# Performance work log

Hardware: AMD Instinct MI355X
Metric: run time of the kernel (lower is better)

The kernel has to match this reference:

```python
import jax, jax.numpy as jnp
import numpy as np

B, S, FEAT = 4, 512, 16
D, H, L, DFF, NC, RPH = 512, 8, 6, 2048, 12, 64
DH = D // H
CLAMP = 5.0
LN_EPS = 1e-5
STD_EPS = 1e-6


def setup_inputs() -> dict:
    key = jax.random.key(0)
    ks = iter(jax.random.split(key, 32))
    sc = lambda *shape: 0.02 * jax.random.normal(next(ks), shape, dtype=jnp.float32)
    inp = {
        "x": jax.random.normal(next(ks), (B, S, FEAT), dtype=jnp.float32),
        # RelPosBias2D MLP: Linear(2,RPH) -> ReLU -> Linear(RPH,H)
        "relpos_w1": sc(RPH, 2), "relpos_b1": jnp.zeros((RPH,), jnp.float32),
        "relpos_w2": sc(H, RPH), "relpos_b2": jnp.zeros((H,), jnp.float32),
        "embed_w": sc(D, FEAT), "embed_b": jnp.zeros((D,), jnp.float32),
        # per-layer params stacked on leading L axis
        "attn_in_w": sc(L, 3 * D, D), "attn_in_b": jnp.zeros((L, 3 * D), jnp.float32),
        "attn_out_w": sc(L, D, D), "attn_out_b": jnp.zeros((L, D), jnp.float32),
        "ff_w1": sc(L, DFF, D), "ff_b1": jnp.zeros((L, DFF), jnp.float32),
        "ff_w2": sc(L, D, DFF), "ff_b2": jnp.zeros((L, D), jnp.float32),
        "ln1_s": jnp.ones((L, D), jnp.float32), "ln1_b": jnp.zeros((L, D), jnp.float32),
        "ln2_s": jnp.ones((L, D), jnp.float32), "ln2_b": jnp.zeros((L, D), jnp.float32),
        "fc_w": sc(NC, D), "fc_b": jnp.zeros((NC,), jnp.float32),
    }
    return inp


def _standardize(v):  # (B,S), unmasked path of _masked_standardize
    mean = v.mean(axis=1, keepdims=True)
    var = ((v - mean) ** 2).mean(axis=1, keepdims=True)
    return (v - mean) / jnp.sqrt(var + STD_EPS)


def _layernorm(v, s, b):
    mean = v.mean(axis=-1, keepdims=True)
    var = ((v - mean) ** 2).mean(axis=-1, keepdims=True)
    return (v - mean) * jax.lax.rsqrt(var + LN_EPS) * s + b


def reference(x, relpos_w1, relpos_b1, relpos_w2, relpos_b2, embed_w, embed_b,
              attn_in_w, attn_in_b, attn_out_w, attn_out_b,
              ff_w1, ff_b1, ff_w2, ff_b2, ln1_s, ln1_b, ln2_s, ln2_b, fc_w, fc_b):
    # --- 2D relative position bias ---
    t = _standardize(x[..., 0])
    f = _standardize(x[..., 1])
    dt = t[:, :, None] - t[:, None, :]          # (B,S,S)
    df = f[:, :, None] - f[:, None, :]
    rel = jnp.stack([dt, df], axis=-1)           # (B,S,S,2)
    hid = jax.nn.relu(rel @ relpos_w1.T + relpos_b1)
    bias = hid @ relpos_w2.T + relpos_b2         # (B,S,S,H)
    bias = jnp.clip(bias, -CLAMP, CLAMP)
    bias = jnp.transpose(bias, (0, 3, 1, 2))     # (B,H,S,S)

    h = x @ embed_w.T + embed_b                  # (B,S,D)
    scale = 1.0 / jnp.sqrt(jnp.float32(DH))
    for l in range(L):
        qkv = h @ attn_in_w[l].T + attn_in_b[l]  # (B,S,3D)
        q, k, v = jnp.split(qkv, 3, axis=-1)
        q = q.reshape(B, S, H, DH)
        k = k.reshape(B, S, H, DH)
        v = v.reshape(B, S, H, DH)
        scores = jnp.einsum('bihd,bjhd->bhij', q, k) * scale + bias
        attn = jax.nn.softmax(scores, axis=-1)
        o = jnp.einsum('bhij,bjhd->bihd', attn, v).reshape(B, S, D)
        o = o @ attn_out_w[l].T + attn_out_b[l]
        h = _layernorm(h + o, ln1_s[l], ln1_b[l])
        ff = jax.nn.relu(h @ ff_w1[l].T + ff_b1[l]) @ ff_w2[l].T + ff_b2[l]
        h = _layernorm(h + ff, ln2_s[l], ln2_b[l])

    rep = h.mean(axis=1)                         # mean pooling, no mask
    return rep @ fc_w.T + fc_b                   # (B,NC)
```

## Files before the change

### kernel.cpp

```cpp
#include <hip/hip_runtime.h>
#include <hip/hip_bf16.h>
#include <stdint.h>

using short8 = __attribute__((ext_vector_type(8))) short;
using us4    = __attribute__((ext_vector_type(4))) unsigned short;
using f32x4  = __attribute__((ext_vector_type(4))) float;
using bf16   = __hip_bfloat16;

constexpr int CB=4, CS=512, CF=16, CD=512, CH=8, CL=6, CDFF=2048, CNC=12, CRPH=64, CDH=64;

__device__ inline void gload_lds16(const void* g, void* l) {
    __builtin_amdgcn_global_load_lds((const __attribute__((address_space(1))) void*)g,
                                     (__attribute__((address_space(3))) void*)l, 16, 0, 0);
}
__device__ inline float bfbits2f(unsigned short u) {
    return __uint_as_float(((uint32_t)u) << 16);
}
__device__ inline unsigned short f2bfbits(float f) {
    return __builtin_bit_cast(unsigned short, __float2bfloat16(f));
}

template<int BM, int BN, int TPB>
struct MMGeom {
    static constexpr int WC  = (TPB == 512) ? 4 : 2;
    static constexpr int WR  = (TPB/64)/WC;
    static constexpr int RS  = BM/WR;
    static constexpr int CSP = BN/WC;
    static constexpr int MR  = RS/16;
    static constexpr int NR  = CSP/16;
    static constexpr int NLD = (BM+BN)*128/(TPB*16);
};

template<int BM, int BN, int TPB>
__device__ inline void stage_tile(const bf16* A, int lda, const bf16* W, int ldw, int k0,
                                  char* As, char* Bs) {
    constexpr int AC = (BM*128)/(TPB*16);
    constexpr int BC = (BN*128)/(TPB*16);
    const int tid = threadIdx.x;
#pragma unroll
    for (int i = 0; i < AC; i++) {
        int s = i*TPB + tid;
        int r = s >> 3, u = s & 7;
        const char* gp = (const char*)(A + (size_t)r*lda + k0) + ((u ^ (r&7))*16);
        gload_lds16(gp, As + (size_t)(s & ~63)*16);
    }
#pragma unroll
    for (int i = 0; i < BC; i++) {
        int s = i*TPB + tid;
        int r = s >> 3, u = s & 7;
        const char* gp = (const char*)(W + (size_t)r*ldw + k0) + ((u ^ (r&7))*16);
        gload_lds16(gp, Bs + (size_t)(s & ~63)*16);
    }
}

template<int BM, int BN, int TPB>
__device__ inline void compute_tile64(const char* As, const char* Bs,
                                      int wr, int wc, int c, int g,
                                      f32x4 (&acc)[MMGeom<BM,BN,TPB>::MR][MMGeom<BM,BN,TPB>::NR]) {
    using G = MMGeom<BM,BN,TPB>;
#pragma unroll
    for (int kk = 0; kk < 2; kk++) {
        short8 af[G::MR], bfv[G::NR];
#pragma unroll
        for (int m = 0; m < G::MR; m++) {
            int row = wr*G::RS + m*16 + c;
            af[m] = *(const short8*)(As + row*128 + (((kk*4+g) ^ (row&7))*16));
        }
#pragma unroll
        for (int n = 0; n < G::NR; n++) {
            int row = wc*G::CSP + n*16 + c;
            bfv[n] = *(const short8*)(Bs + row*128 + (((kk*4+g) ^ (row&7))*16));
        }
#pragma unroll
        for (int m = 0; m < G::MR; m++)
#pragma unroll
            for (int n = 0; n < G::NR; n++)
                acc[m][n] = __builtin_amdgcn_mfma_f32_16x16x32_bf16(af[m], bfv[n], acc[m][n], 0, 0, 0);
    }
}

template<int BM, int BN, int TPB>
__device__ inline void mm_core_pipe(const bf16* A, int lda, const bf16* W, int ldw, int K,
                                    char* smem,
                                    f32x4 (&acc)[MMGeom<BM,BN,TPB>::MR][MMGeom<BM,BN,TPB>::NR]) {
    using G = MMGeom<BM,BN,TPB>;
    constexpr int SSZ = (BM+BN)*128;
    const int tid = threadIdx.x;
    const int lane = tid & 63, wv = tid >> 6;
    const int wr = wv / G::WC, wc = wv % G::WC;
    const int g = lane >> 4, c = lane & 15;

    const int nk = K >> 6;
    stage_tile<BM,BN,TPB>(A, lda, W, ldw, 0, smem, smem + BM*128);
    if (nk > 1) stage_tile<BM,BN,TPB>(A, lda, W, ldw, 64, smem + SSZ, smem + SSZ + BM*128);

    for (int t = 0; t < nk; t++) {
        char* bc = smem + (size_t)(t & 3)*SSZ;
        if (t + 2 < nk) {
            char* bs = smem + (size_t)((t+2) & 3)*SSZ;
            stage_tile<BM,BN,TPB>(A, lda, W, ldw, (t+2)*64, bs, bs + BM*128);
            asm volatile("s_waitcnt vmcnt(%0)" :: "n"(2*G::NLD) : "memory");
        } else if (t + 1 < nk) {
            asm volatile("s_waitcnt vmcnt(%0)" :: "n"(G::NLD) : "memory");
        } else {
            asm volatile("s_waitcnt vmcnt(0)" ::: "memory");
        }
        __builtin_amdgcn_s_barrier();
        compute_tile64<BM,BN,TPB>(bc, bc + BM*128, wr, wc, c, g, acc);
    }
}

template<int BM, int BN, int EPI, int KSPLIT, int TPB>
__global__ __launch_bounds__(TPB) void k_mm(const bf16* __restrict__ A, int lda,
                                            const bf16* __restrict__ W, int ldw,
                                            const float* __restrict__ bias,
                                            bf16* __restrict__ Cb, float* __restrict__ Cf,
                                            int ldc, int K) {
    using G = MMGeom<BM,BN,TPB>;
    __shared__ char smem[4*(BM+BN)*128];
    const int bm = blockIdx.y * BM, bn = blockIdx.x * BN;
    const int kz = (KSPLIT > 1) ? blockIdx.z : 0;
    const int Kper = K / KSPLIT;
    f32x4 acc[G::MR][G::NR] = {};
    mm_core_pipe<BM,BN,TPB>(A + (size_t)bm*lda + kz*Kper, lda,
                            W + (size_t)bn*ldw + kz*Kper, ldw, Kper, smem, acc);
    const int lane = threadIdx.x & 63, wv = threadIdx.x >> 6;
    const int wr = wv / G::WC, wc = wv % G::WC;
    const int g = lane >> 4, c = lane & 15;
    float* Cfz = Cf + (size_t)kz * 2048 * ldc;
#pragma unroll
    for (int m = 0; m < G::MR; m++)
#pragma unroll
        for (int n = 0; n < G::NR; n++)
#pragma unroll
            for (int j = 0; j < 4; j++) {
                int row = bm + wr*G::RS + m*16 + g*4 + j;
                int col = bn + wc*G::CSP + n*16 + c;
                float v = acc[m][n][j] + ((kz == 0) ? bias[col] : 0.0f);
                if (EPI == 1) v = fmaxf(v, 0.0f);
                if (EPI == 2) Cfz[(size_t)row*ldc + col] = v;
                else          Cb[(size_t)row*ldc + col] = __float2bfloat16(v);
            }
}

__global__ __launch_bounds__(512) void k_mm_qkv(const bf16* __restrict__ A,
                                                const bf16* __restrict__ W,
                                                const float* __restrict__ bias,
                                                bf16* __restrict__ qkvb,
                                                bf16* __restrict__ vtb) {
    constexpr int BM = 128, BN = 128, TPB = 512;
    using G = MMGeom<BM,BN,TPB>;
    __shared__ char smem[4*(BM+BN)*128];
    const int bm = blockIdx.y * BM, bn = blockIdx.x * BN;
    f32x4 acc[G::MR][G::NR] = {};
    mm_core_pipe<BM,BN,TPB>(A + (size_t)bm*CD, CD, W + (size_t)bn*CD, CD, CD, smem, acc);
    const int lane = threadIdx.x & 63, wv = threadIdx.x >> 6;
    const int wr = wv / G::WC, wc = wv % G::WC;
    const int g = lane >> 4, c = lane & 15;
    if (bn < 2*CD) {
#pragma unroll
        for (int m = 0; m < G::MR; m++)
#pragma unroll
            for (int n = 0; n < G::NR; n++)
#pragma unroll
                for (int j = 0; j < 4; j++) {
                    int row = bm + wr*G::RS + m*16 + g*4 + j;
                    int col = bn + wc*G::CSP + n*16 + c;
                    qkvb[(size_t)row*(3*CD) + col] = __float2bfloat16(acc[m][n][j] + bias[col]);
                }
    } else {
#pragma unroll
        for (int m = 0; m < G::MR; m++)
#pragma unroll
            for (int n = 0; n < G::NR; n++) {
                int row0 = bm + wr*G::RS + m*16 + g*4;
                int col  = bn + wc*G::CSP + n*16 + c;
                int z = (row0 >> 9)*8 + ((col - 2*CD) >> 6);
                int d = (col - 2*CD) & 63;
                int s0 = row0 & 511;
                float bcol = bias[col];
                us4 o;
#pragma unroll
                for (int j = 0; j < 4; j++) o[j] = f2bfbits(acc[m][n][j] + bcol);
                *(us4*)(vtb + ((size_t)z*CDH + d)*CS + s0) = o;
            }
    }
}

__global__ __launch_bounds__(256) void k_attn_fused(const bf16* __restrict__ qkv,
                                                    const bf16* __restrict__ vt,
                                                    const bf16* __restrict__ bias,
                                                    bf16* __restrict__ att) {
    __shared__ char Ksm[4][16384];
    __shared__ char Vsm[4][16384];
    __shared__ char Ps[16384];

    const int z = blockIdx.y, b = z >> 3, h = z & 7;
    const int qbase = blockIdx.x * 64;
    const int tid = threadIdx.x, l = tid & 63, w = tid >> 6;
    const int g = l >> 4, c = l & 15, swz = l & 7;
    const int q_global = qbase + w*16 + c;

    const bf16* qrow = qkv + ((size_t)(b*CS + q_global))*(3*CD) + h*CDH;
    short8 bq0 = *(const short8*)(qrow + g*8);
    short8 bq1 = *(const short8*)(qrow + 32 + g*8);
    const bf16* brow = bias + ((size_t)z*CS + q_global)*CS;

    float mrun = -1e30f, lsum = 0.0f;
    f32x4 accO[4] = {};
    char* Pb = Ps + w*4096;

    auto stageKV = [&](int kv0, char* Ks, char* Vs) {
#pragma unroll
        for (int i = 0; i < 4; i++) {
            int s = i*256 + tid;
            int r = s >> 3, u = s & 7;
            const bf16* gk = qkv + ((size_t)(b*CS + kv0 + r))*(3*CD) + CD + h*CDH + ((u ^ (r&7)) * 8);
            gload_lds16(gk, Ks + (size_t)(s & ~63)*16);
        }
#pragma unroll
        for (int i = 0; i < 4; i++) {
            int s = i*256 + tid;
            int d = s >> 4, u = s & 15;
            const bf16* gv = vt + ((size_t)(z*CDH + d))*CS + kv0 + ((u ^ (d&7)) * 8);
            gload_lds16(gv, Vs + (size_t)(s & ~63)*16);
        }
    };

    stageKV(0,   Ksm[0], Vsm[0]);
    stageKV(128, Ksm[1], Vsm[1]);

    for (int t = 0; t < 4; t++) {
        int kv0 = t * 128;
        if (t < 2) stageKV((t+2)*128, Ksm[t+2], Vsm[t+2]);
        if (t == 0)      asm volatile("s_waitcnt vmcnt(32)" ::: "memory");
        else if (t == 1) asm volatile("s_waitcnt vmcnt(40)" ::: "memory");
        else if (t == 2) asm volatile("s_waitcnt vmcnt(32)" ::: "memory");
        else             asm volatile("s_waitcnt vmcnt(16)" ::: "memory");
        __builtin_amdgcn_s_barrier();
        const char* Kc = Ksm[t];
        const char* Vc = Vsm[t];

        float sv[8][4];
        float tmax = -1e30f;
#pragma unroll
        for (int n = 0; n < 8; n++) {
            int row = n*16 + c;
            short8 af0 = *(const short8*)(Kc + row*128 + ((g    ^ swz) * 16));
            short8 af1 = *(const short8*)(Kc + row*128 + (((4+g) ^ swz) * 16));
            f32x4 a = {};
            a = __builtin_amdgcn_mfma_f32_16x16x32_bf16(af0, bq0, a, 0, 0, 0);
            a = __builtin_amdgcn_mfma_f32_16x16x32_bf16(af1, bq1, a, 0, 0, 0);
            us4 b4 = *(const us4*)(brow + kv0 + n*16 + g*4);
#pragma unroll
            for (int j = 0; j < 4; j++) {
                sv[n][j] = a[j] * 0.125f + bfbits2f(b4[j]);
                tmax = fmaxf(tmax, sv[n][j]);
            }
        }
        tmax = fmaxf(tmax, __shfl_xor(tmax, 16));
        tmax = fmaxf(tmax, __shfl_xor(tmax, 32));
        if (!__all(tmax - mrun <= 8.0f)) {
            float mnew = fmaxf(mrun, tmax);
            float corr = __expf(mrun - mnew);
            lsum *= corr;
#pragma unroll
            for (int n2 = 0; n2 < 4; n2++)
#pragma unroll
                for (int j = 0; j < 4; j++) accO[n2][j] *= corr;
            mrun = mnew;
        }
        float tsum = 0.0f;
#pragma unroll
        for (int n = 0; n < 8; n++)
#pragma unroll
            for (int j = 0; j < 4; j++) {
                float e = __expf(sv[n][j] - mrun);
                sv[n][j] = e;
                tsum += e;
            }
        tsum += __shfl_xor(tsum, 16);
        tsum += __shfl_xor(tsum, 32);
        lsum += tsum;

#pragma unroll
        for (int n = 0; n < 8; n++) {
            us4 pk;
#pragma unroll
            for (int j = 0; j < 4; j++) pk[j] = f2bfbits(sv[n][j]);
            *(us4*)(Pb + c*256 + ((n*32 + g*8) ^ (swz << 4))) = pk;
        }

#pragma unroll
        for (int n2 = 0; n2 < 4; n2++) {
            int d = n2*16 + c;
#pragma unroll
            for (int kk = 0; kk < 4; kk++) {
                short8 av = *(const short8*)(Vc + d*256 + (((kk*4 + g) ^ swz) * 16));
                short8 bp = *(const short8*)(Pb + c*256 + (((kk*64 + g*16) ^ (swz << 4))));
                accO[n2] = __builtin_amdgcn_mfma_f32_16x16x32_bf16(av, bp, accO[n2], 0, 0, 0);
            }
        }
    }

    float inv = 1.0f / lsum;
    bf16* orow = att + ((size_t)(b*CS + q_global))*CD + h*CDH;
#pragma unroll
    for (int n2 = 0; n2 < 4; n2++) {
        us4 o;
#pragma unroll
        for (int j = 0; j < 4; j++) o[j] = f2bfbits(accO[n2][j] * inv);
        *(us4*)(orow + n2*16 + g*4) = o;
    }
}

__global__ void k_standardize(const float* __restrict__ x, float* __restrict__ ts,
                              float* __restrict__ fs) {
    int b = blockIdx.x, ch = blockIdx.y, tid = threadIdx.x;
    __shared__ float red[256];
    float v0 = x[(b*CS + tid)*CF + ch];
    float v1 = x[(b*CS + tid + 256)*CF + ch];
    red[tid] = v0 + v1; __syncthreads();
    for (int w = 128; w > 0; w >>= 1) { if (tid < w) red[tid] += red[tid+w]; __syncthreads(); }
    float mean = red[0] * (1.0f/CS); __syncthreads();
    float d0 = v0-mean, d1 = v1-mean;
    red[tid] = d0*d0 + d1*d1; __syncthreads();
    for (int w = 128; w > 0; w >>= 1) { if (tid < w) red[tid] += red[tid+w]; __syncthreads(); }
    float inv = rsqrtf(red[0]*(1.0f/CS) + 1e-6f);
    float* o = ch == 0 ? ts : fs;
    o[b*CS + tid] = d0*inv; o[b*CS + tid + 256] = d1*inv;
}

__global__ __launch_bounds__(256) void k_relpos(const float* __restrict__ ts, const float* __restrict__ fs,
                         const float* __restrict__ w1, const float* __restrict__ b1,
                         const float* __restrict__ w2, const float* __restrict__ b2,
                         bf16* __restrict__ bias) {
    int idx = blockIdx.x * 256 + threadIdx.x;
    int j = idx & (CS-1), i = (idx >> 9) & (CS-1), b = idx >> 18;
    float dt = ts[b*CS + i] - ts[b*CS + j];
    float df = fs[b*CS + i] - fs[b*CS + j];
    float acc[CH];
#pragma unroll
    for (int h = 0; h < CH; h++) acc[h] = b2[h];
    for (int r = 0; r < CRPH; r++) {
        float hd = fmaxf(w1[r*2]*dt + w1[r*2+1]*df + b1[r], 0.0f);
#pragma unroll
        for (int h = 0; h < CH; h++) acc[h] += w2[h*CRPH + r] * hd;
    }
#pragma unroll
    for (int h = 0; h < CH; h++) {
        float v = fminf(fmaxf(acc[h], -5.0f), 5.0f);
        bias[((size_t)(b*CH + h)*CS + i)*CS + j] = __float2bfloat16(v);
    }
}

__global__ __launch_bounds__(256) void k_embed(const float* __restrict__ x, const float* __restrict__ w,
                        const float* __restrict__ bv, float* __restrict__ h, bf16* __restrict__ hb) {
    int idx = blockIdx.x * 256 + threadIdx.x;
    int d = idx & (CD-1), m = idx >> 9;
    const float* xr = x + m*CF;
    const float* wr = w + d*CF;
    float acc = bv[d];
#pragma unroll
    for (int f = 0; f < CF; f++) acc += xr[f]*wr[f];
    h[idx] = acc; hb[idx] = __float2bfloat16(acc);
}

template<int NADD>
__global__ __launch_bounds__(256) void k_ln(float* __restrict__ h, const float* __restrict__ a0,
                     const float* __restrict__ a1,
                     const float* __restrict__ s, const float* __restrict__ bv, bf16* __restrict__ hb) {
    const int w = threadIdx.x >> 6, l = threadIdx.x & 63;
    const int row = blockIdx.x*4 + w;
    float* hr = h + (size_t)row*CD;
    const float* ar = a0 + (size_t)row*CD;
    const float* a1r = (NADD == 2) ? (a1 + (size_t)row*CD) : nullptr;

    float v[8];
    {
        float4 h0 = ((const float4*)hr)[l*2],  h1 = ((const float4*)hr)[l*2+1];
        float4 b0 = ((const float4*)ar)[l*2],  b1 = ((const float4*)ar)[l*2+1];
        v[0]=h0.x+b0.x; v[1]=h0.y+b0.y; v[2]=h0.z+b0.z; v[3]=h0.w+b0.w;
        v[4]=h1.x+b1.x; v[5]=h1.y+b1.y; v[6]=h1.z+b1.z; v[7]=h1.w+b1.w;
        if (NADD == 2) {
            float4 c0 = ((const float4*)a1r)[l*2], c1 = ((const float4*)a1r)[l*2+1];
            v[0]+=c0.x; v[1]+=c0.y; v[2]+=c0.z; v[3]+=c0.w;
            v[4]+=c1.x; v[5]+=c1.y; v[6]+=c1.z; v[7]+=c1.w;
        }
    }
    float sum = 0.f, sq = 0.f;
#pragma unroll
    for (int i = 0; i < 8; i++) { sum += v[i]; sq += v[i]*v[i]; }
#pragma unroll
    for (int off = 1; off < 64; off <<= 1) {
        sum += __shfl_xor(sum, off);
        sq  += __shfl_xor(sq, off);
    }
    float mean = sum * (1.0f/CD);
    float var  = sq * (1.0f/CD) - mean*mean;
    float rstd = rsqrtf(var + 1e-5f);

    float4 s0 = ((const float4*)s)[l*2],  s1 = ((const float4*)s)[l*2+1];
    float4 g0 = ((const float4*)bv)[l*2], g1 = ((const float4*)bv)[l*2+1];
    float o[8];
    o[0]=(v[0]-mean)*rstd*s0.x+g0.x; o[1]=(v[1]-mean)*rstd*s0.y+g0.y;
    o[2]=(v[2]-mean)*rstd*s0.z+g0.z; o[3]=(v[3]-mean)*rstd*s0.w+g0.w;
    o[4]=(v[4]-mean)*rstd*s1.x+g1.x; o[5]=(v[5]-mean)*rstd*s1.y+g1.y;
    o[6]=(v[6]-mean)*rstd*s1.z+g1.z; o[7]=(v[7]-mean)*rstd*s1.w+g1.w;

    ((float4*)hr)[l*2]   = make_float4(o[0],o[1],o[2],o[3]);
    ((float4*)hr)[l*2+1] = make_float4(o[4],o[5],o[6],o[7]);
    short8 ob;
#pragma unroll
    for (int i = 0; i < 8; i++) ob[i] = (short)f2bfbits(o[i]);
    *(short8*)(hb + (size_t)row*CD + l*8) = ob;
}

__global__ __launch_bounds__(256) void k_wconv(const float* __restrict__ a0, const float* __restrict__ a1,
                        const float* __restrict__ a2, const float* __restrict__ a3,
                        bf16* __restrict__ dst) {
    size_t i = ((size_t)blockIdx.x * 256 + threadIdx.x) * 8;
    const float* src; size_t off;
    if (i < 786432)       { src = a0; off = i; }
    else if (i < 1048576) { src = a1; off = i - 786432; }
    else if (i < 2097152) { src = a2; off = i - 1048576; }
    else                  { src = a3; off = i - 2097152; }
    short8 o;
#pragma unroll
    for (int j = 0; j < 8; j++) o[j] = __builtin_bit_cast(short, __float2bfloat16(src[off + j]));
    *(short8*)(void*)(dst + i) = o;
}

__global__ __launch_bounds__(256) void k_wconv_all(const float* __restrict__ aiw, const float* __restrict__ aow,
                        const float* __restrict__ f1w, const float* __restrict__ f2w,
                        bf16* __restrict__ dst) {
    int lyr = blockIdx.y;
    size_t i = ((size_t)blockIdx.x * 256 + threadIdx.x) * 8;
    const float* src; size_t off;
    if (i < 786432)       { src = aiw + (size_t)lyr* 786432; off = i; }
    else if (i < 1048576) { src = aow + (size_t)lyr* 262144; off = i - 786432; }
    else if (i < 2097152) { src = f1w + (size_t)lyr*1048576; off = i - 1048576; }
    else                  { src = f2w + (size_t)lyr*1048576; off = i - 2097152; }
    short8 o;
#pragma unroll
    for (int j = 0; j < 8; j++) o[j] = __builtin_bit_cast(short, __float2bfloat16(src[off + j]));
    *(short8*)(void*)(dst + (size_t)lyr*3145728 + i) = o;
}

__global__ __launch_bounds__(256) void k_pool(const float* __restrict__ h, float* __restrict__ rep) {
    int b = blockIdx.x, d0 = blockIdx.y * 64;
    int t = threadIdx.x, dl = t & 63, sg = t >> 6;
    float acc = 0.0f;
    for (int s = sg*128; s < sg*128 + 128; s++)
        acc += h[((size_t)(b*CS + s))*CD + d0 + dl];
    __shared__ float red[256];
    red[t] = acc; __syncthreads();
    if (t < 64)
        rep[b*CD + d0 + dl] = (red[t] + red[t+64] + red[t+128] + red[t+192]) * (1.0f/CS);
}

__global__ void k_fc(const float* __restrict__ rep, const float* __restrict__ fcw,
                     const float* __restrict__ fcb, float* __restrict__ out) {
    int b = blockIdx.x, cc = blockIdx.y, l = threadIdx.x;
    float acc = 0.0f;
    for (int d = l; d < CD; d += 64) acc += rep[b*CD + d] * fcw[cc*CD + d];
    for (int o = 32; o > 0; o >>= 1) acc += __shfl_xor(acc, o);
    if (l == 0) out[b*CNC + cc] = acc + fcb[cc];
}

extern "C" void kernel_launch(void* const* d_in, const int* in_sizes, int n_in,
                              void* d_out, int out_size, void* d_ws, size_t ws_size,
                              hipStream_t stream) {
    const float* x   = (const float*)d_in[0];
    const float* rw1 = (const float*)d_in[1];
    const float* rb1 = (const float*)d_in[2];
    const float* rw2 = (const float*)d_in[3];
    const float* rb2 = (const float*)d_in[4];
    const float* emw = (const float*)d_in[5];
    const float* emb = (const float*)d_in[6];
    const float* aiw = (const float*)d_in[7];
    const float* aib = (const float*)d_in[8];
    const float* aow = (const float*)d_in[9];
    const float* aob = (const float*)d_in[10];
    const float* f1w = (const float*)d_in[11];
    const float* f1b = (const float*)d_in[12];
    const float* f2w = (const float*)d_in[13];
    const float* f2b = (const float*)d_in[14];
    const float* l1s = (const float*)d_in[15];
    const float* l1b = (const float*)d_in[16];
    const float* l2s = (const float*)d_in[17];
    const float* l2b = (const float*)d_in[18];
    const float* fcw = (const float*)d_in[19];
    const float* fcb = (const float*)d_in[20];
    float* out = (float*)d_out;

    char* p = (char*)d_ws;
    auto alloc = [&](size_t bytes) { char* r = p; p += (bytes + 255) & ~(size_t)255; return r; };
    bf16*  biasb = (bf16*)alloc((size_t)CB*CH*CS*CS*2);
    float* h     = (float*)alloc((size_t)CB*CS*CD*4);
    bf16*  hb    = (bf16*)alloc((size_t)CB*CS*CD*2);
    bf16*  qkvb  = (bf16*)alloc((size_t)CB*CS*3*CD*2);
    bf16*  vtb   = (bf16*)alloc((size_t)CB*CH*CDH*CS*2);
    bf16*  attb  = (bf16*)alloc((size_t)CB*CS*CD*2);
    float* tmp   = (float*)alloc((size_t)2*CB*CS*CD*4);
    bf16*  ffb   = (bf16*)alloc((size_t)CB*CS*CDFF*2);
    bf16*  wl    = (bf16*)alloc((size_t)3145728*2);
    float* rep   = (float*)alloc((size_t)CB*CD*4);
    float* ts    = (float*)alloc(CB*CS*4);
    float* fs    = (float*)alloc(CB*CS*4);

    size_t used = (size_t)(p - (char*)d_ws);
    const size_t WLE = 3145728;
    bool oneshot = (ws_size > used) && ((ws_size - used) >= (size_t)CL*WLE*2 + 256);
    bf16* wlall = (bf16*)alloc(oneshot ? (size_t)CL*WLE*2 : 0);

    const int M = CB*CS;
    float* tmp2 = tmp + (size_t)M*CD;

    k_standardize<<<dim3(CB,2), 256, 0, stream>>>(x, ts, fs);
    k_relpos<<<(CB*CS*CS)/256, 256, 0, stream>>>(ts, fs, rw1, rb1, rw2, rb2, biasb);
    k_embed<<<(M*CD)/256, 256, 0, stream>>>(x, emw, emb, h, hb);
    if (oneshot)
        k_wconv_all<<<dim3(1536, CL), 256, 0, stream>>>(aiw, aow, f1w, f2w, wlall);

    for (int l = 0; l < CL; l++) {
        const bf16* wbase = oneshot ? (wlall + (size_t)l*WLE) : wl;
        if (!oneshot)
            k_wconv<<<1536, 256, 0, stream>>>(aiw + (size_t)l*786432, aow + (size_t)l*262144,
                                              f1w + (size_t)l*1048576, f2w + (size_t)l*1048576, wl);
        const bf16* wl_aiw = wbase;
        const bf16* wl_aow = wbase + 786432;
        const bf16* wl_f1w = wbase + 1048576;
        const bf16* wl_f2w = wbase + 2097152;
        k_mm_qkv<<<dim3(12,16), 512, 0, stream>>>(hb, wl_aiw, aib + (size_t)l*3*CD, qkvb, vtb);
        k_attn_fused<<<dim3(CS/64, CB*CH), 256, 0, stream>>>(qkvb, vtb, biasb, attb);
        k_mm<64,64,2,1,512><<<dim3(8,32), 512, 0, stream>>>(attb, CD, wl_aow, CD,
                                                            aob + (size_t)l*CD, nullptr, tmp, CD, CD);
        k_ln<1><<<M/4, 256, 0, stream>>>(h, tmp, nullptr, l1s + (size_t)l*CD, l1b + (size_t)l*CD, hb);
        k_mm<128,128,1,1,512><<<dim3(16,16), 512, 0, stream>>>(hb, CD, wl_f1w, CD,
                                                               f1b + (size_t)l*CDFF, ffb, nullptr, CDFF, CD);
        k_mm<64,64,2,2,512><<<dim3(8,32,2), 512, 0, stream>>>(ffb, CDFF, wl_f2w, CDFF,
                                                              f2b + (size_t)l*CD, nullptr, tmp, CD, CDFF);
        k_ln<2><<<M/4, 256, 0, stream>>>(h, tmp, tmp2, l2s + (size_t)l*CD, l2b + (size_t)l*CD, hb);
    }

    k_pool<<<dim3(CB, CD/64), 256, 0, stream>>>(h, rep);
    k_fc<<<dim3(CB, CNC), 64, 0, stream>>>(rep, fcw, fcb, out);
}
```

Measured before the change: 457.8 us.

## Rework GEMM tiling to 256-thread blocks with double buffering and fuse pool+fc

The GEMM kernels switch from 512-thread blocks with a 4-stage LDS ring to 256-thread blocks in which every wave covers all rows, using a double-buffered pipeline with a barrier after each compute step. Tile shapes change: QKV and FF1 use 64x128 tiles, and the attention-output projection gains a K-split of 2 with its reduction folded into layernorm. The attention wait count is tightened to vmcnt(0), and pooling and the final linear layer are merged into one kernel. These changes alter occupancy and launch count, but the shallower prefetch and extra barriers may expose more memory latency.

```diff
diff --git a/kernel.cpp b/kernel.cpp
--- a/kernel.cpp
+++ b/kernel.cpp
@@ -8,6 +8,7 @@
 using bf16   = __hip_bfloat16;
 
 constexpr int CB=4, CS=512, CF=16, CD=512, CH=8, CL=6, CDFF=2048, CNC=12, CRPH=64, CDH=64;
+constexpr int MROWS = CB*CS;
 
 __device__ inline void gload_lds16(const void* g, void* l) {
     __builtin_amdgcn_global_load_lds((const __attribute__((address_space(1))) void*)g,
@@ -20,50 +21,47 @@
     return __builtin_bit_cast(unsigned short, __float2bfloat16(f));
 }
 
-template<int BM, int BN, int TPB>
-struct MMGeom {
-    static constexpr int WC  = (TPB == 512) ? 4 : 2;
-    static constexpr int WR  = (TPB/64)/WC;
-    static constexpr int RS  = BM/WR;
-    static constexpr int CSP = BN/WC;
-    static constexpr int MR  = RS/16;
+template<int BM, int BN>
+struct MMG {
+    static constexpr int CSP = BN/4;
+    static constexpr int MR  = BM/16;
     static constexpr int NR  = CSP/16;
-    static constexpr int NLD = (BM+BN)*128/(TPB*16);
+    static constexpr int NLD = (BM+BN)*128/(256*16);
 };
 
-template<int BM, int BN, int TPB>
+template<int BM, int BN>
 __device__ inline void stage_tile(const bf16* A, int lda, const bf16* W, int ldw, int k0,
                                   char* As, char* Bs) {
-    constexpr int AC = (BM*128)/(TPB*16);
-    constexpr int BC = (BN*128)/(TPB*16);
+    constexpr int AC = (BM*128)/(256*16);
+    constexpr int BC = (BN*128)/(256*16);
     const int tid = threadIdx.x;
 #pragma unroll
     for (int i = 0; i < AC; i++) {
-        int s = i*TPB + tid;
+        int s = i*256 + tid;
         int r = s >> 3, u = s & 7;
         const char* gp = (const char*)(A + (size_t)r*lda + k0) + ((u ^ (r&7))*16);
         gload_lds16(gp, As + (size_t)(s & ~63)*16);
     }
 #pragma unroll
     for (int i = 0; i < BC; i++) {
-        int s = i*TPB + tid;
+        int s = i*256 + tid;
         int r = s >> 3, u = s & 7;
         const char* gp = (const char*)(W + (size_t)r*ldw + k0) + ((u ^ (r&7))*16);
         gload_lds16(gp, Bs + (size_t)(s & ~63)*16);
     }
 }
 
-template<int BM, int BN, int TPB>
+template<int BM, int BN>
 __device__ inline void compute_tile64(const char* As, const char* Bs,
-                                      int wr, int wc, int c, int g,
-                                      f32x4 (&acc)[MMGeom<BM,BN,TPB>::MR][MMGeom<BM,BN,TPB>::NR]) {
-    using G = MMGeom<BM,BN,TPB>;
+                                      int wc, int c, int g,
+                                      f32x4 (&acc)[MMG<BM,BN>::MR][MMG<BM,BN>::NR]) {
+    using G = MMG<BM,BN>;
 #pragma unroll
     for (int kk = 0; kk < 2; kk++) {
         short8 af[G::MR], bfv[G::NR];
 #pragma unroll
         for (int m = 0; m < G::MR; m++) {
-            int row = wr*G::RS + m*16 + c;
+            int row = m*16 + c;
             af[m] = *(const short8*)(As + row*128 + (((kk*4+g) ^ (row&7))*16));
         }
 #pragma unroll
@@ -79,63 +77,57 @@
     }
 }
 
-template<int BM, int BN, int TPB>
+template<int BM, int BN>
 __device__ inline void mm_core_pipe(const bf16* A, int lda, const bf16* W, int ldw, int K,
                                     char* smem,
-                                    f32x4 (&acc)[MMGeom<BM,BN,TPB>::MR][MMGeom<BM,BN,TPB>::NR]) {
-    using G = MMGeom<BM,BN,TPB>;
+                                    f32x4 (&acc)[MMG<BM,BN>::MR][MMG<BM,BN>::NR]) {
+    using G = MMG<BM,BN>;
     constexpr int SSZ = (BM+BN)*128;
-    const int tid = threadIdx.x;
-    const int lane = tid & 63, wv = tid >> 6;
-    const int wr = wv / G::WC, wc = wv % G::WC;
+    const int lane = threadIdx.x & 63, wv = threadIdx.x >> 6;
     const int g = lane >> 4, c = lane & 15;
 
     const int nk = K >> 6;
-    stage_tile<BM,BN,TPB>(A, lda, W, ldw, 0, smem, smem + BM*128);
-    if (nk > 1) stage_tile<BM,BN,TPB>(A, lda, W, ldw, 64, smem + SSZ, smem + SSZ + BM*128);
-
+    stage_tile<BM,BN>(A, lda, W, ldw, 0, smem, smem + BM*128);
     for (int t = 0; t < nk; t++) {
-        char* bc = smem + (size_t)(t & 3)*SSZ;
-        if (t + 2 < nk) {
-            char* bs = smem + (size_t)((t+2) & 3)*SSZ;
-            stage_tile<BM,BN,TPB>(A, lda, W, ldw, (t+2)*64, bs, bs + BM*128);
-            asm volatile("s_waitcnt vmcnt(%0)" :: "n"(2*G::NLD) : "memory");
-        } else if (t + 1 < nk) {
+        char* bc = smem + (size_t)(t & 1)*SSZ;
+        if (t + 1 < nk) {
+            char* bs = smem + (size_t)((t+1) & 1)*SSZ;
+            stage_tile<BM,BN>(A, lda, W, ldw, (t+1)*64, bs, bs + BM*128);
             asm volatile("s_waitcnt vmcnt(%0)" :: "n"(G::NLD) : "memory");
         } else {
             asm volatile("s_waitcnt vmcnt(0)" ::: "memory");
         }
         __builtin_amdgcn_s_barrier();
-        compute_tile64<BM,BN,TPB>(bc, bc + BM*128, wr, wc, c, g, acc);
-    }
-}
-
-template<int BM, int BN, int EPI, int KSPLIT, int TPB>
-__global__ __launch_bounds__(TPB) void k_mm(const bf16* __restrict__ A, int lda,
+        compute_tile64<BM,BN>(bc, bc + BM*128, wv, c, g, acc);
+        __builtin_amdgcn_s_barrier();
+    }
+}
+
+template<int BM, int BN, int EPI, int KSPLIT>
+__global__ __launch_bounds__(256) void k_mm(const bf16* __restrict__ A, int lda,
                                             const bf16* __restrict__ W, int ldw,
                                             const float* __restrict__ bias,
                                             bf16* __restrict__ Cb, float* __restrict__ Cf,
                                             int ldc, int K) {
-    using G = MMGeom<BM,BN,TPB>;
-    __shared__ char smem[4*(BM+BN)*128];
+    using G = MMG<BM,BN>;
+    __shared__ char smem[2*(BM+BN)*128];
     const int bm = blockIdx.y * BM, bn = blockIdx.x * BN;
     const int kz = (KSPLIT > 1) ? blockIdx.z : 0;
     const int Kper = K / KSPLIT;
     f32x4 acc[G::MR][G::NR] = {};
-    mm_core_pipe<BM,BN,TPB>(A + (size_t)bm*lda + kz*Kper, lda,
-                            W + (size_t)bn*ldw + kz*Kper, ldw, Kper, smem, acc);
+    mm_core_pipe<BM,BN>(A + (size_t)bm*lda + kz*Kper, lda,
+                        W + (size_t)bn*ldw + kz*Kper, ldw, Kper, smem, acc);
     const int lane = threadIdx.x & 63, wv = threadIdx.x >> 6;
-    const int wr = wv / G::WC, wc = wv % G::WC;
     const int g = lane >> 4, c = lane & 15;
-    float* Cfz = Cf + (size_t)kz * 2048 * ldc;
+    float* Cfz = Cf + (size_t)kz * MROWS * ldc;
 #pragma unroll
     for (int m = 0; m < G::MR; m++)
 #pragma unroll
         for (int n = 0; n < G::NR; n++)
 #pragma unroll
             for (int j = 0; j < 4; j++) {
-                int row = bm + wr*G::RS + m*16 + g*4 + j;
-                int col = bn + wc*G::CSP + n*16 + c;
+                int row = bm + m*16 + g*4 + j;
+                int col = bn + wv*G::CSP + n*16 + c;
                 float v = acc[m][n][j] + ((kz == 0) ? bias[col] : 0.0f);
                 if (EPI == 1) v = fmaxf(v, 0.0f);
                 if (EPI == 2) Cfz[(size_t)row*ldc + col] = v;
@@ -143,19 +135,18 @@
             }
 }
 
-__global__ __launch_bounds__(512) void k_mm_qkv(const bf16* __restrict__ A,
+__global__ __launch_bounds__(256) void k_mm_qkv(const bf16* __restrict__ A,
                                                 const bf16* __restrict__ W,
                                                 const float* __restrict__ bias,
                                                 bf16* __restrict__ qkvb,
                                                 bf16* __restrict__ vtb) {
-    constexpr int BM = 128, BN = 128, TPB = 512;
-    using G = MMGeom<BM,BN,TPB>;
-    __shared__ char smem[4*(BM+BN)*128];
+    constexpr int BM = 64, BN = 128;
+    using G = MMG<BM,BN>;
+    __shared__ char smem[2*(BM+BN)*128];
     const int bm = blockIdx.y * BM, bn = blockIdx.x * BN;
     f32x4 acc[G::MR][G::NR] = {};
-    mm_core_pipe<BM,BN,TPB>(A + (size_t)bm*CD, CD, W + (size_t)bn*CD, CD, CD, smem, acc);
+    mm_core_pipe<BM,BN>(A + (size_t)bm*CD, CD, W + (size_t)bn*CD, CD, CD, smem, acc);
     const int lane = threadIdx.x & 63, wv = threadIdx.x >> 6;
-    const int wr = wv / G::WC, wc = wv % G::WC;
     const int g = lane >> 4, c = lane & 15;
     if (bn < 2*CD) {
 #pragma unroll
@@ -164,8 +155,8 @@
             for (int n = 0; n < G::NR; n++)
 #pragma unroll
                 for (int j = 0; j < 4; j++) {
-                    int row = bm + wr*G::RS + m*16 + g*4 + j;
-                    int col = bn + wc*G::CSP + n*16 + c;
+                    int row = bm + m*16 + g*4 + j;
+                    int col = bn + wv*G::CSP + n*16 + c;
                     qkvb[(size_t)row*(3*CD) + col] = __float2bfloat16(acc[m][n][j] + bias[col]);
                 }
     } else {
@@ -173,8 +164,8 @@
         for (int m = 0; m < G::MR; m++)
 #pragma unroll
             for (int n = 0; n < G::NR; n++) {
-                int row0 = bm + wr*G::RS + m*16 + g*4;
-                int col  = bn + wc*G::CSP + n*16 + c;
+                int row0 = bm + m*16 + g*4;
+                int col  = bn + wv*G::CSP + n*16 + c;
                 int z = (row0 >> 9)*8 + ((col - 2*CD) >> 6);
                 int d = (col - 2*CD) & 63;
                 int s0 = row0 & 511;
@@ -236,7 +227,7 @@
         if (t == 0)      asm volatile("s_waitcnt vmcnt(32)" ::: "memory");
         else if (t == 1) asm volatile("s_waitcnt vmcnt(40)" ::: "memory");
         else if (t == 2) asm volatile("s_waitcnt vmcnt(32)" ::: "memory");
-        else             asm volatile("s_waitcnt vmcnt(16)" ::: "memory");
+        else             asm volatile("s_waitcnt vmcnt(0)" ::: "memory");
         __builtin_amdgcn_s_barrier();
         const char* Kc = Ksm[t];
         const char* Vc = Vsm[t];
@@ -416,21 +407,6 @@
     *(short8*)(hb + (size_t)row*CD + l*8) = ob;
 }
 
-__global__ __launch_bounds__(256) void k_wconv(const float* __restrict__ a0, const float* __restrict__ a1,
-                        const float* __restrict__ a2, const float* __restrict__ a3,
-                        bf16* __restrict__ dst) {
-    size_t i = ((size_t)blockIdx.x * 256 + threadIdx.x) * 8;
-    const float* src; size_t off;
-    if (i < 786432)       { src = a0; off = i; }
-    else if (i < 1048576) { src = a1; off = i - 786432; }
-    else if (i < 2097152) { src = a2; off = i - 1048576; }
-    else                  { src = a3; off = i - 2097152; }
-    short8 o;
-#pragma unroll
-    for (int j = 0; j < 8; j++) o[j] = __builtin_bit_cast(short, __float2bfloat16(src[off + j]));
-    *(short8*)(void*)(dst + i) = o;
-}
-
 __global__ __launch_bounds__(256) void k_wconv_all(const float* __restrict__ aiw, const float* __restrict__ aow,
                         const float* __restrict__ f1w, const float* __restrict__ f2w,
                         bf16* __restrict__ dst) {
@@ -447,25 +423,43 @@
     *(short8*)(void*)(dst + (size_t)lyr*3145728 + i) = o;
 }
 
-__global__ __launch_bounds__(256) void k_pool(const float* __restrict__ h, float* __restrict__ rep) {
-    int b = blockIdx.x, d0 = blockIdx.y * 64;
-    int t = threadIdx.x, dl = t & 63, sg = t >> 6;
-    float acc = 0.0f;
-    for (int s = sg*128; s < sg*128 + 128; s++)
-        acc += h[((size_t)(b*CS + s))*CD + d0 + dl];
-    __shared__ float red[256];
-    red[t] = acc; __syncthreads();
-    if (t < 64)
-        rep[b*CD + d0 + dl] = (red[t] + red[t+64] + red[t+128] + red[t+192]) * (1.0f/CS);
-}
-
-__global__ void k_fc(const float* __restrict__ rep, const float* __restrict__ fcw,
-                     const float* __restrict__ fcb, float* __restrict__ out) {
-    int b = blockIdx.x, cc = blockIdx.y, l = threadIdx.x;
-    float acc = 0.0f;
-    for (int d = l; d < CD; d += 64) acc += rep[b*CD + d] * fcw[cc*CD + d];
-    for (int o = 32; o > 0; o >>= 1) acc += __shfl_xor(acc, o);
-    if (l == 0) out[b*CNC + cc] = acc + fcb[cc];
+__global__ __launch_bounds__(256) void k_wconv(const float* __restrict__ a0, const float* __restrict__ a1,
+                        const float* __restrict__ a2, const float* __restrict__ a3,
+                        bf16* __restrict__ dst) {
+    size_t i = ((size_t)blockIdx.x * 256 + threadIdx.x) * 8;
+    const float* src; size_t off;
+    if (i < 786432)       { src = a0; off = i; }
+    else if (i < 1048576) { src = a1; off = i - 786432; }
+    else if (i < 2097152) { src = a2; off = i - 1048576; }
+    else                  { src = a3; off = i - 2097152; }
+    short8 o;
+#pragma unroll
+    for (int j = 0; j < 8; j++) o[j] = __builtin_bit_cast(short, __float2bfloat16(src[off + j]));
+    *(short8*)(void*)(dst + i) = o;
+}
+
+__global__ __launch_bounds__(256) void k_poolfc(const float* __restrict__ h,
+                                                const float* __restrict__ fcw,
+                                                const float* __restrict__ fcb,
+                                                float* __restrict__ out) {
+    __shared__ float rep[CD];
+    int b = blockIdx.x, t = threadIdx.x;
+    float a0 = 0.f, a1 = 0.f;
+    for (int s = 0; s < CS; s++) {
+        const float* row = h + (size_t)(b*CS + s)*CD;
+        a0 += row[t];
+        a1 += row[t + 256];
+    }
+    rep[t] = a0 * (1.0f/CS);
+    rep[t + 256] = a1 * (1.0f/CS);
+    __syncthreads();
+    int w = t >> 6, l = t & 63;
+    for (int cc = w*3; cc < w*3 + 3 && cc < CNC; cc++) {
+        float acc = 0.f;
+        for (int d = l; d < CD; d += 64) acc += rep[d] * fcw[cc*CD + d];
+        for (int o = 32; o > 0; o >>= 1) acc += __shfl_xor(acc, o);
+        if (l == 0) out[b*CNC + cc] = acc + fcb[cc];
+    }
 }
 
 extern "C" void kernel_launch(void* const* d_in, const int* in_sizes, int n_in,
@@ -497,15 +491,14 @@
     char* p = (char*)d_ws;
     auto alloc = [&](size_t bytes) { char* r = p; p += (bytes + 255) & ~(size_t)255; return r; };
     bf16*  biasb = (bf16*)alloc((size_t)CB*CH*CS*CS*2);
-    float* h     = (float*)alloc((size_t)CB*CS*CD*4);
-    bf16*  hb    = (bf16*)alloc((size_t)CB*CS*CD*2);
-    bf16*  qkvb  = (bf16*)alloc((size_t)CB*CS*3*CD*2);
+    float* h     = (float*)alloc((size_t)MROWS*CD*4);
+    bf16*  hb    = (bf16*)alloc((size_t)MROWS*CD*2);
+    bf16*  qkvb  = (bf16*)alloc((size_t)MROWS*3*CD*2);
     bf16*  vtb   = (bf16*)alloc((size_t)CB*CH*CDH*CS*2);
-    bf16*  attb  = (bf16*)alloc((size_t)CB*CS*CD*2);
-    float* tmp   = (float*)alloc((size_t)2*CB*CS*CD*4);
-    bf16*  ffb   = (bf16*)alloc((size_t)CB*CS*CDFF*2);
+    bf16*  attb  = (bf16*)alloc((size_t)MROWS*CD*2);
+    float* tmp   = (float*)alloc((size_t)2*MROWS*CD*4);
+    bf16*  ffb   = (bf16*)alloc((size_t)MROWS*CDFF*2);
     bf16*  wl    = (bf16*)alloc((size_t)3145728*2);
-    float* rep   = (float*)alloc((size_t)CB*CD*4);
     float* ts    = (float*)alloc(CB*CS*4);
     float* fs    = (float*)alloc(CB*CS*4);
 
@@ -514,7 +507,7 @@
     bool oneshot = (ws_size > used) && ((ws_size - used) >= (size_t)CL*WLE*2 + 256);
     bf16* wlall = (bf16*)alloc(oneshot ? (size_t)CL*WLE*2 : 0);
 
-    const int M = CB*CS;
+    const int M = MROWS;
     float* tmp2 = tmp + (size_t)M*CD;
 
     k_standardize<<<dim3(CB,2), 256, 0, stream>>>(x, ts, fs);
@@ -532,18 +525,18 @@
         const bf16* wl_aow = wbase + 786432;
         const bf16* wl_f1w = wbase + 1048576;
         const bf16* wl_f2w = wbase + 2097152;
-        k_mm_qkv<<<dim3(12,16), 512, 0, stream>>>(hb, wl_aiw, aib + (size_t)l*3*CD, qkvb, vtb);
+
+        k_mm_qkv<<<dim3(12, 32), 256, 0, stream>>>(hb, wl_aiw, aib + (size_t)l*3*CD, qkvb, vtb);
         k_attn_fused<<<dim3(CS/64, CB*CH), 256, 0, stream>>>(qkvb, vtb, biasb, attb);
-        k_mm<64,64,2,1,512><<<dim3(8,32), 512, 0, stream>>>(attb, CD, wl_aow, CD,
-                                                            aob + (size_t)l*CD, nullptr, tmp, CD, CD);
-        k_ln<1><<<M/4, 256, 0, stream>>>(h, tmp, nullptr, l1s + (size_t)l*CD, l1b + (size_t)l*CD, hb);
-        k_mm<128,128,1,1,512><<<dim3(16,16), 512, 0, stream>>>(hb, CD, wl_f1w, CD,
-                                                               f1b + (size_t)l*CDFF, ffb, nullptr, CDFF, CD);
-        k_mm<64,64,2,2,512><<<dim3(8,32,2), 512, 0, stream>>>(ffb, CDFF, wl_f2w, CDFF,
-                                                              f2b + (size_t)l*CD, nullptr, tmp, CD, CDFF);
+        k_mm<64,64,2,2><<<dim3(8,32,2), 256, 0, stream>>>(attb, CD, wl_aow, CD,
+                                                          aob + (size_t)l*CD, nullptr, tmp, CD, CD);
+        k_ln<2><<<M/4, 256, 0, stream>>>(h, tmp, tmp2, l1s + (size_t)l*CD, l1b + (size_t)l*CD, hb);
+        k_mm<64,128,1,1><<<dim3(16,32), 256, 0, stream>>>(hb, CD, wl_f1w, CD,
+                                                          f1b + (size_t)l*CDFF, ffb, nullptr, CDFF, CD);
+        k_mm<64,64,2,2><<<dim3(8,32,2), 256, 0, stream>>>(ffb, CDFF, wl_f2w, CDFF,
+                                                          f2b + (size_t)l*CD, nullptr, tmp, CD, CDFF);
         k_ln<2><<<M/4, 256, 0, stream>>>(h, tmp, tmp2, l2s + (size_t)l*CD, l2b + (size_t)l*CD, hb);
     }
 
-    k_pool<<<dim3(CB, CD/64), 256, 0, stream>>>(h, rep);
-    k_fc<<<dim3(CB, CNC), 64, 0, stream>>>(rep, fcw, fcb, out);
-}
+    k_poolfc<<<CB, 256, 0, stream>>>(h, fcw, fcb, out);
+}
```

Result: no change. 465.0 us (+1.6%).
